# Optimization experiments

Measured on AMD Instinct MI355X. Metric: run time of the kernel, lower is better.

The kernel has to match this reference:

```python
import jax, jax.numpy as jnp
import numpy as np

B, S, DM, H, NSYN = 4, 2048, 768, 12, 4
HD = DM // H  # 64
EPS = 1e-12
SCALE = float(DM / H) ** -0.5  # 1/sqrt(head_dim)


def setup_inputs() -> dict:
    key = jax.random.key(0)
    ks = jax.random.split(key, 16)
    p = 0.02
    return {
        "hidden_states": jax.random.normal(ks[0], (B, S, DM), jnp.float32),
        "attention_mask": jnp.zeros((B, 1, 1, S), jnp.float32),
        "addi_key": jax.random.normal(ks[1], (B, NSYN, S, HD), jnp.float32),
        "addi_value": jax.random.normal(ks[2], (B, NSYN, S, HD), jnp.float32),
        "Wq": jax.random.normal(ks[3], (DM, DM), jnp.float32) * p,
        "bq": jnp.zeros((DM,), jnp.float32),
        "Wk": jax.random.normal(ks[4], (DM, DM), jnp.float32) * p,
        "bk": jnp.zeros((DM,), jnp.float32),
        "Wv": jax.random.normal(ks[5], (DM, DM), jnp.float32) * p,
        "bv": jnp.zeros((DM,), jnp.float32),
        "Wo": jax.random.normal(ks[6], (DM, DM), jnp.float32) * p,
        "bo": jnp.zeros((DM,), jnp.float32),
        "ln_g": jnp.ones((DM,), jnp.float32),
        "ln_b": jnp.zeros((DM,), jnp.float32),
    }


def _heads(x):
    # [B,S,DM] -> [B,H,S,HD]
    return x.reshape(B, S, H, HD).transpose(0, 2, 1, 3)


def reference(hidden_states, attention_mask, addi_key, addi_value,
              Wq, bq, Wk, bk, Wv, bv, Wo, bo, ln_g, ln_b):
    x = hidden_states
    q = _heads(jnp.einsum('bsi,oi->bso', x, Wq) + bq)
    k = _heads(jnp.einsum('bsi,oi->bso', x, Wk) + bk)
    v = _heads(jnp.einsum('bsi,oi->bso', x, Wv) + bv)
    # additive key/value injection on first NSYN heads
    k = k.at[:, :NSYN].add(addi_key)
    v = v.at[:, :NSYN].add(addi_value)
    scores = jnp.einsum('bhqd,bhkd->bhqk', q, k) * SCALE + attention_mask
    probs = jax.nn.softmax(scores, axis=-1)
    ctx = jnp.einsum('bhqk,bhkd->bhqd', probs, v)
    ctx = ctx.transpose(0, 2, 1, 3).reshape(B, S, DM)
    out = jnp.einsum('bsi,oi->bso', ctx, Wo) + bo
    h = out + x  # residual
    mu = jnp.mean(h, axis=-1, keepdims=True)
    var = jnp.mean((h - mu) ** 2, axis=-1, keepdims=True)
    return (h - mu) * jax.lax.rsqrt(var + EPS) * ln_g + ln_b
```

## Files before the change

kernel.cpp:

```cpp
#include <hip/hip_runtime.h>


typedef __bf16 bf16;
typedef __bf16 bf16x8 __attribute__((ext_vector_type(8)));
typedef __bf16 bf16x4 __attribute__((ext_vector_type(4)));
typedef float floatx4 __attribute__((ext_vector_type(4)));
typedef unsigned int uint2v __attribute__((ext_vector_type(2)));

#define BB 4
#define SS 2048
#define DM 768
#define HH 12
#define HD 64
#define NSYN 4
#define MM (BB*SS)
#define KK DM
#define SCALE 0.125f
#define LOG2E 1.4426950408889634f
#define QSCALE (SCALE * LOG2E)

#define N_X   ((size_t)MM * DM)
#define N_W   ((size_t)DM * DM)
#define N_M   ((size_t)BB * SS)

#if __has_builtin(__builtin_amdgcn_exp2f)
#define EXP2(x) __builtin_amdgcn_exp2f(x)
#else
#define EXP2(x) exp2f(x)
#endif

#define ASYNC16(gp, lp)                                                        \
    __builtin_amdgcn_global_load_lds(                                          \
        (const __attribute__((address_space(1))) unsigned int*)(gp),           \
        (__attribute__((address_space(3))) unsigned int*)(lp), 16, 0, 0)

static __device__ __forceinline__ void pl32_swap(unsigned int& a, unsigned int& b) {
#if __has_builtin(__builtin_amdgcn_permlane32_swap)
    uint2v r = __builtin_amdgcn_permlane32_swap(a, b, false, false);
    a = r[0]; b = r[1];
#else
    asm volatile("v_permlane32_swap_b32 %0, %1" : "+v"(a), "+v"(b));
#endif
}
static __device__ __forceinline__ void pl16_swap(unsigned int& a, unsigned int& b) {
#if __has_builtin(__builtin_amdgcn_permlane16_swap)
    uint2v r = __builtin_amdgcn_permlane16_swap(a, b, false, false);
    a = r[0]; b = r[1];
#else
    asm volatile("v_permlane16_swap_b32 %0, %1" : "+v"(a), "+v"(b));
#endif
}

__global__ __launch_bounds__(256) void cvt_kernel(
    const float* __restrict__ x,
    const float* __restrict__ Wq, const float* __restrict__ Wk,
    const float* __restrict__ Wv, const float* __restrict__ Wo,
    const float* __restrict__ mask,
    bf16* __restrict__ xb,
    bf16* __restrict__ Wqb, bf16* __restrict__ Wkb,
    bf16* __restrict__ Wvb, bf16* __restrict__ Wob,
    float* __restrict__ ml2e)
{
    const size_t nx4 = N_X / 4, nw4 = N_W / 4, nm4 = N_M / 4;
    size_t i = (size_t)blockIdx.x * blockDim.x + threadIdx.x;
    if (i >= nx4 + 4 * nw4) {
        size_t off = i - nx4 - 4 * nw4;
        if (off < nm4) {
            float4 m = *(const float4*)(mask + off * 4);
            float4 o = { m.x * LOG2E, m.y * LOG2E, m.z * LOG2E, m.w * LOG2E };
            *(float4*)(ml2e + off * 4) = o;
        }
        return;
    }
    const float* src; bf16* dst; size_t off;
    if (i < nx4)                { src = x;  dst = xb;  off = i; }
    else if (i < nx4 + nw4)     { src = Wq; dst = Wqb; off = i - nx4; }
    else if (i < nx4 + 2*nw4)   { src = Wk; dst = Wkb; off = i - nx4 - nw4; }
    else if (i < nx4 + 3*nw4)   { src = Wv; dst = Wvb; off = i - nx4 - 2*nw4; }
    else                        { src = Wo; dst = Wob; off = i - nx4 - 3*nw4; }
    float4 v = *(const float4*)(src + off * 4);
    bf16x4 o = { (bf16)v.x, (bf16)v.y, (bf16)v.z, (bf16)v.w };
    *(bf16x4*)(dst + off * 4) = o;
}

template<int ORD>
__device__ __forceinline__ void gemm_ml128_bk64(
    const bf16* __restrict__ A, const bf16* __restrict__ Bw,
    int tileM, bf16* As, bf16* Bs, floatx4 acc[2][8])
{
    const int tid  = threadIdx.x;
    const int lane = tid & 63;
    const int wave = tid >> 6;
    const int l15 = lane & 15, quad = lane >> 4;

    const int sr  = wave * 32 + (lane >> 3);
    const int scl = (lane & 7) ^ ((lane >> 3) & 7);
    const bf16* gA = A  + (size_t)(tileM * 128 + sr) * KK + scl * 8;
    const bf16* gB = Bw + (size_t)sr * KK + scl * 8;
    bf16* lA = As + (wave * 32) * 64;
    bf16* lB = Bs + (wave * 32) * 64;

    #pragma unroll
    for (int g = 0; g < 4; ++g) {
        ASYNC16(gA + (size_t)(g * 8) * KK, lA + g * 512);
        ASYNC16(gB + (size_t)(g * 8) * KK, lB + g * 512);
    }
    __syncthreads();

    for (int kt = 0; kt < KK / 64; ++kt) {
        const int cur = kt & 1;
        if (kt + 1 < KK / 64) {
            const int nb = (1 - cur) * 8192;
            #pragma unroll
            for (int g = 0; g < 4; ++g) {
                ASYNC16(gA + (kt + 1) * 64 + (size_t)(g * 8) * KK, lA + nb + g * 512);
                ASYNC16(gB + (kt + 1) * 64 + (size_t)(g * 8) * KK, lB + nb + g * 512);
            }
        }
        const bf16* cA = As + cur * 8192;
        const bf16* cB = Bs + cur * 8192;
        #pragma unroll
        for (int c = 0; c < 2; ++c) {
            const int pc = (4 * c + quad) ^ (l15 & 7);
            bf16x8 af[2];
            #pragma unroll
            for (int i = 0; i < 2; ++i)
                af[i] = *(const bf16x8*)(cA + (wave * 32 + i * 16 + l15) * 64 + pc * 8);
            #pragma unroll
            for (int j = 0; j < 8; ++j) {
                bf16x8 bfr = *(const bf16x8*)(cB + (j * 16 + l15) * 64 + pc * 8);
                #pragma unroll
                for (int i = 0; i < 2; ++i)
                    acc[i][j] = (ORD == 0)
                        ? __builtin_amdgcn_mfma_f32_16x16x32_bf16(af[i], bfr, acc[i][j], 0, 0, 0)
                        : __builtin_amdgcn_mfma_f32_16x16x32_bf16(bfr, af[i], acc[i][j], 0, 0, 0);
            }
        }
        __syncthreads();
    }
}

template<int ORD>
__device__ __forceinline__ void gemm_ml64_bk64(
    const bf16* __restrict__ A, const bf16* __restrict__ Bw,
    int tileM, int tileN, bf16* As, bf16* Bs, floatx4 acc[2][4])
{
    const int tid  = threadIdx.x;
    const int lane = tid & 63;
    const int wave = tid >> 6;
    const int l15 = lane & 15, quad = lane >> 4;

    const int srA = wave * 32 + (lane >> 3);
    const int srB = wave * 16 + (lane >> 3);
    const int scl = (lane & 7) ^ ((lane >> 3) & 7);
    const bf16* gA = A  + (size_t)(tileM * 128 + srA) * KK + scl * 8;
    const bf16* gB = Bw + (size_t)(tileN *  64 + srB) * KK + scl * 8;
    bf16* lA = As + (wave * 32) * 64;
    bf16* lB = Bs + (wave * 16) * 64;

    #pragma unroll
    for (int g = 0; g < 4; ++g) ASYNC16(gA + (size_t)(g * 8) * KK, lA + g * 512);
    #pragma unroll
    for (int g = 0; g < 2; ++g) ASYNC16(gB + (size_t)(g * 8) * KK, lB + g * 512);
    __syncthreads();

    for (int kt = 0; kt < KK / 64; ++kt) {
        const int cur = kt & 1;
        if (kt + 1 < KK / 64) {
            const int nbA = (1 - cur) * 8192;
            const int nbB = (1 - cur) * 4096;
            #pragma unroll
            for (int g = 0; g < 4; ++g)
                ASYNC16(gA + (kt + 1) * 64 + (size_t)(g * 8) * KK, lA + nbA + g * 512);
            #pragma unroll
            for (int g = 0; g < 2; ++g)
                ASYNC16(gB + (kt + 1) * 64 + (size_t)(g * 8) * KK, lB + nbB + g * 512);
        }
        const bf16* cA = As + cur * 8192;
        const bf16* cB = Bs + cur * 4096;
        #pragma unroll
        for (int c = 0; c < 2; ++c) {
            const int pc = (4 * c + quad) ^ (l15 & 7);
            bf16x8 af[2];
            #pragma unroll
            for (int i = 0; i < 2; ++i)
                af[i] = *(const bf16x8*)(cA + (wave * 32 + i * 16 + l15) * 64 + pc * 8);
            #pragma unroll
            for (int j = 0; j < 4; ++j) {
                bf16x8 bfr = *(const bf16x8*)(cB + (j * 16 + l15) * 64 + pc * 8);
                #pragma unroll
                for (int i = 0; i < 2; ++i)
                    acc[i][j] = (ORD == 0)
                        ? __builtin_amdgcn_mfma_f32_16x16x32_bf16(af[i], bfr, acc[i][j], 0, 0, 0)
                        : __builtin_amdgcn_mfma_f32_16x16x32_bf16(bfr, af[i], acc[i][j], 0, 0, 0);
            }
        }
        __syncthreads();
    }
}

__global__ __launch_bounds__(256, 2) void qkv_kernel(
    const bf16* __restrict__ xb,
    const bf16* __restrict__ Wqb, const float* __restrict__ bq,
    const bf16* __restrict__ Wkb, const float* __restrict__ bk,
    const bf16* __restrict__ Wvb, const float* __restrict__ bv,
    const float* __restrict__ addi_key, const float* __restrict__ addi_value,
    bf16* __restrict__ qbuf, bf16* __restrict__ kbuf, bf16* __restrict__ vtbuf)
{
    __shared__ __align__(16) bf16 As[2 * 128 * 64];
    __shared__ __align__(16) bf16 Bs[2 * 128 * 64];
    const int u = blockIdx.x;
    const int tileM = u & 63;
    const int tileN = u >> 6;
    const int z     = tileN / 6;
    const int tN    = tileN % 6;
    const bf16* W     = (z == 0) ? Wqb : (z == 1) ? Wkb : Wvb;
    const float* bias = (z == 0) ? bq  : (z == 1) ? bk  : bv;
    const bf16* Wrow  = W + (size_t)(tN * 128) * KK;

    floatx4 acc[2][8];
    #pragma unroll
    for (int i = 0; i < 2; ++i)
        #pragma unroll
        for (int j = 0; j < 8; ++j) { floatx4 zv = {0.f, 0.f, 0.f, 0.f}; acc[i][j] = zv; }

    const int lane = threadIdx.x & 63, wave = threadIdx.x >> 6;
    const int l15 = lane & 15, quad = lane >> 4;

    if (z == 2) {
        gemm_ml128_bk64<0>(xb, Wrow, tileM, As, Bs, acc);
        #pragma unroll
        for (int i = 0; i < 2; ++i) {
            const int sg0 = tileM * 128 + wave * 32 + i * 16 + quad * 4;
            const int b = sg0 >> 11, s0 = sg0 & 2047;
            #pragma unroll
            for (int j = 0; j < 8; ++j) {
                const int o = tN * 128 + j * 16 + l15;
                const float bv_ = bias[o];
                const int h = o >> 6, d = o & 63;
                float vv[4];
                #pragma unroll
                for (int rr = 0; rr < 4; ++rr) {
                    vv[rr] = acc[i][j][rr] + bv_;
                    if (h < NSYN)
                        vv[rr] += addi_value[(((size_t)b * NSYN + h) * SS + s0 + rr) * HD + d];
                }
                bf16x4 pk = { (bf16)vv[0], (bf16)vv[1], (bf16)vv[2], (bf16)vv[3] };
                *(bf16x4*)(vtbuf + (((size_t)b * HH + h) * HD + d) * SS + s0) = pk;
            }
        }
    } else {
        gemm_ml128_bk64<1>(xb, Wrow, tileM, As, Bs, acc);
        #pragma unroll
        for (int i = 0; i < 2; ++i) {
            const int sg = tileM * 128 + wave * 32 + i * 16 + l15;
            const int b = sg >> 11, s = sg & 2047;
            #pragma unroll
            for (int j = 0; j < 8; ++j) {
                const int o0 = tN * 128 + j * 16 + quad * 4;
                const int h = o0 >> 6, d0 = o0 & 63;
                float4 b4 = *(const float4*)(bias + o0);
                float vv[4] = { acc[i][j][0] + b4.x, acc[i][j][1] + b4.y,
                                acc[i][j][2] + b4.z, acc[i][j][3] + b4.w };
                if (z == 1 && h < NSYN) {
                    float4 a4 = *(const float4*)(addi_key +
                        (((size_t)b * NSYN + h) * SS + s) * HD + d0);
                    vv[0] += a4.x; vv[1] += a4.y; vv[2] += a4.z; vv[3] += a4.w;
                }
                if (z == 0) {
                    bf16x4 pk = { (bf16)(vv[0] * QSCALE), (bf16)(vv[1] * QSCALE),
                                  (bf16)(vv[2] * QSCALE), (bf16)(vv[3] * QSCALE) };
                    *(bf16x4*)(qbuf + (((size_t)b * HH + h) * SS + s) * HD + d0) = pk;
                } else {
                    bf16x4 pk = { (bf16)vv[0], (bf16)vv[1], (bf16)vv[2], (bf16)vv[3] };
                    *(bf16x4*)(kbuf + (((size_t)b * HH + h) * SS + s) * HD + d0) = pk;
                }
            }
        }
    }
}

__global__ __launch_bounds__(256, 3) void attn_kernel(
    const bf16* __restrict__ qbuf, const bf16* __restrict__ kbuf,
    const bf16* __restrict__ vtbuf, const float* __restrict__ ml2e,
    bf16* __restrict__ ctx)
{
    __shared__ __align__(16) bf16 Ks[2 * 64 * 64];
    __shared__ __align__(16) bf16 Vt[2 * 64 * 64];

    const int u  = blockIdx.x;
    const int bh = u % 48;
    const int qt = u / 48;
    const int b  = bh / 12;
    const int h  = bh % 12;
    const size_t bhs = ((size_t)b * HH + h) * SS * HD;
    const int tid = threadIdx.x, lane = tid & 63, wave = tid >> 6;
    const int l15 = lane & 15, quad = lane >> 4;
    const int q0 = qt * 128 + wave * 32;

    const int sr  = wave * 16 + (lane >> 3);
    const int scl = (lane & 7) ^ ((lane >> 3) & 7);
    const bf16* gK = kbuf  + bhs + (size_t)sr * HD + scl * 8;
    const bf16* gV = vtbuf + bhs + (size_t)sr * SS + scl * 8;
    bf16* lK = Ks + (wave * 16) * 64;
    bf16* lV = Vt + (wave * 16) * 64;

    bf16x8 qf[2][2];
    #pragma unroll
    for (int n = 0; n < 2; ++n)
        #pragma unroll
        for (int c = 0; c < 2; ++c)
            qf[n][c] = *(const bf16x8*)(qbuf + bhs +
                (size_t)(q0 + n * 16 + l15) * HD + c * 32 + quad * 8);

    bf16x8 ones;
    #pragma unroll
    for (int e = 0; e < 8; ++e) ones[e] = (bf16)1.0f;

    floatx4 acco[2][4];
    #pragma unroll
    for (int n = 0; n < 2; ++n)
        #pragma unroll
        for (int t = 0; t < 4; ++t) { floatx4 zv = {0.f, 0.f, 0.f, 0.f}; acco[n][t] = zv; }
    floatx4 lacc[2];
    { floatx4 zv = {0.f, 0.f, 0.f, 0.f}; lacc[0] = zv; lacc[1] = zv; }

    const float* mb = ml2e + (size_t)b * SS;

    #pragma unroll
    for (int p = 0; p < 2; ++p) {
        ASYNC16(gK + (size_t)p * 8 * HD,  lK + p * 512);
        ASYNC16(gV + (size_t)p * 8 * SS,  lV + p * 512);
    }
    __syncthreads();

    for (int kt = 0; kt < SS / 64; ++kt) {
        float4 mk4[4];
        #pragma unroll
        for (int j = 0; j < 4; ++j)
            mk4[j] = *(const float4*)(mb + kt * 64 + j * 16 + quad * 4);

        const int cur = kt & 1;
        if (kt + 1 < SS / 64) {
            const int nb = (1 - cur) * 4096;
            #pragma unroll
            for (int p = 0; p < 2; ++p) {
                ASYNC16(gK + ((size_t)(kt + 1) * 64 + p * 8) * HD, lK + nb + p * 512);
                ASYNC16(gV + (size_t)p * 8 * SS + (kt + 1) * 64,   lV + nb + p * 512);
            }
        }
        const bf16* cK = Ks + cur * 4096;
        const bf16* cV = Vt + cur * 4096;

        floatx4 sacc[2][4];
        #pragma unroll
        for (int j = 0; j < 4; ++j) {
            floatx4 mv = { mk4[j].x, mk4[j].y, mk4[j].z, mk4[j].w };
            sacc[0][j] = mv;
            sacc[1][j] = mv;
        }
        __builtin_amdgcn_s_setprio(1);
        #pragma unroll
        for (int c = 0; c < 2; ++c) {
            const int pc = (4 * c + quad) ^ (l15 & 7);
            #pragma unroll
            for (int j = 0; j < 4; ++j) {
                bf16x8 af = *(const bf16x8*)(cK + (j * 16 + l15) * 64 + pc * 8);
                #pragma unroll
                for (int n = 0; n < 2; ++n)
                    sacc[n][j] = __builtin_amdgcn_mfma_f32_16x16x32_bf16(af, qf[n][c], sacc[n][j], 0, 0, 0);
            }
        }
        __builtin_amdgcn_s_setprio(0);

        unsigned int w[2][4][2];
        #pragma unroll
        for (int j = 0; j < 4; ++j) {
            #pragma unroll
            for (int n = 0; n < 2; ++n) {
                float p0 = EXP2(sacc[n][j][0]);
                float p1 = EXP2(sacc[n][j][1]);
                float p2 = EXP2(sacc[n][j][2]);
                float p3 = EXP2(sacc[n][j][3]);
                union { bf16x4 v; unsigned int u2[2]; } pk;
                pk.v = (bf16x4){ (bf16)p0, (bf16)p1, (bf16)p2, (bf16)p3 };
                w[n][j][0] = pk.u2[0];
                w[n][j][1] = pk.u2[1];
            }
        }
        #pragma unroll
        for (int n = 0; n < 2; ++n) {
            pl32_swap(w[n][0][0], w[n][1][0]);  pl32_swap(w[n][0][1], w[n][1][1]);
            pl32_swap(w[n][2][0], w[n][3][0]);  pl32_swap(w[n][2][1], w[n][3][1]);
        }
        #pragma unroll
        for (int n = 0; n < 2; ++n) {
            pl16_swap(w[n][0][0], w[n][1][0]);  pl16_swap(w[n][0][1], w[n][1][1]);
            pl16_swap(w[n][2][0], w[n][3][0]);  pl16_swap(w[n][2][1], w[n][3][1]);
        }
        union { unsigned int u2[4]; bf16x8 v; } pb[2][2];
        #pragma unroll
        for (int n = 0; n < 2; ++n) {
            pb[n][0].u2[0] = w[n][0][0]; pb[n][0].u2[1] = w[n][0][1];
            pb[n][0].u2[2] = w[n][1][0]; pb[n][0].u2[3] = w[n][1][1];
            pb[n][1].u2[0] = w[n][2][0]; pb[n][1].u2[1] = w[n][2][1];
            pb[n][1].u2[2] = w[n][3][0]; pb[n][1].u2[3] = w[n][3][1];
        }

        __builtin_amdgcn_s_setprio(1);
        #pragma unroll
        for (int c = 0; c < 2; ++c) {
            const int pc = (4 * c + quad) ^ (l15 & 7);
            #pragma unroll
            for (int n = 0; n < 2; ++n)
                lacc[n] = __builtin_amdgcn_mfma_f32_16x16x32_bf16(ones, pb[n][c].v, lacc[n], 0, 0, 0);
            #pragma unroll
            for (int t = 0; t < 4; ++t) {
                bf16x8 af = *(const bf16x8*)(cV + (t * 16 + l15) * 64 + pc * 8);
                #pragma unroll
                for (int n = 0; n < 2; ++n)
                    acco[n][t] = __builtin_amdgcn_mfma_f32_16x16x32_bf16(af, pb[n][c].v, acco[n][t], 0, 0, 0);
            }
        }
        __builtin_amdgcn_s_setprio(0);
        __syncthreads();
    }

    #pragma unroll
    for (int n = 0; n < 2; ++n) {
        const float inv = 1.0f / lacc[n][0];
        bf16* crow = ctx + ((size_t)(b * SS + q0 + n * 16 + l15)) * DM + h * HD;
        #pragma unroll
        for (int t = 0; t < 4; ++t) {
            bf16x4 ov = { (bf16)(acco[n][t][0] * inv), (bf16)(acco[n][t][1] * inv),
                          (bf16)(acco[n][t][2] * inv), (bf16)(acco[n][t][3] * inv) };
            *(bf16x4*)(crow + t * 16 + quad * 4) = ov;
        }
    }
}

__global__ __launch_bounds__(256, 3) void oproj_kernel(
    const bf16* __restrict__ ctx, const bf16* __restrict__ Wob,
    const float* __restrict__ bo, const float* __restrict__ x,
    bf16* __restrict__ hbuf)
{
    __shared__ __align__(16) bf16 As[2 * 128 * 64];
    __shared__ __align__(16) bf16 Bs[2 * 64 * 64];
    const int u = blockIdx.x;
    const int tileM = u & 63;
    const int tileN = u >> 6;

    floatx4 acc[2][4];
    #pragma unroll
    for (int i = 0; i < 2; ++i)
        #pragma unroll
        for (int j = 0; j < 4; ++j) { floatx4 zv = {0.f, 0.f, 0.f, 0.f}; acc[i][j] = zv; }

    gemm_ml64_bk64<1>(ctx, Wob, tileM, tileN, As, Bs, acc);

    const int lane = threadIdx.x & 63, wave = threadIdx.x >> 6;
    const int l15 = lane & 15, quad = lane >> 4;
    #pragma unroll
    for (int i = 0; i < 2; ++i) {
        const int sg = tileM * 128 + wave * 32 + i * 16 + l15;
        #pragma unroll
        for (int j = 0; j < 4; ++j) {
            const int o0 = tileN * 64 + j * 16 + quad * 4;
            float4 b4 = *(const float4*)(bo + o0);
            float4 r4 = *(const float4*)(x + (size_t)sg * DM + o0);
            bf16x4 pk = { (bf16)(acc[i][j][0] + b4.x + r4.x),
                          (bf16)(acc[i][j][1] + b4.y + r4.y),
                          (bf16)(acc[i][j][2] + b4.z + r4.z),
                          (bf16)(acc[i][j][3] + b4.w + r4.w) };
            *(bf16x4*)(hbuf + (size_t)sg * DM + o0) = pk;
        }
    }
}

__global__ __launch_bounds__(256) void ln_kernel(
    const bf16* __restrict__ hbuf, const float* __restrict__ g,
    const float* __restrict__ be, float* __restrict__ out)
{
    const int row  = blockIdx.x * 4 + (threadIdx.x >> 6);
    const int lane = threadIdx.x & 63;
    const bf16* hr = hbuf + (size_t)row * DM;

    bf16x8 va = *(const bf16x8*)(hr + lane * 8);
    bf16x4 vb = *(const bf16x4*)(hr + 512 + lane * 4);
    float v[12];
    #pragma unroll
    for (int i = 0; i < 8; ++i) v[i] = (float)va[i];
    #pragma unroll
    for (int i = 0; i < 4; ++i) v[8 + i] = (float)vb[i];

    float s = 0.f;
    #pragma unroll
    for (int i = 0; i < 12; ++i) s += v[i];
    #pragma unroll
    for (int m = 1; m < 64; m <<= 1) s += __shfl_xor(s, m);
    const float mu = s * (1.0f / DM);

    float s2 = 0.f;
    #pragma unroll
    for (int i = 0; i < 12; ++i) { v[i] -= mu; s2 += v[i] * v[i]; }
    #pragma unroll
    for (int m = 1; m < 64; m <<= 1) s2 += __shfl_xor(s2, m);
    const float rsv = rsqrtf(s2 * (1.0f / DM) + 1e-12f);

    float* orow = out + (size_t)row * DM;
    const int c0 = lane * 8, c1 = 512 + lane * 4;
    float4 g0 = *(const float4*)(g + c0),     g1 = *(const float4*)(g + c0 + 4);
    float4 g2 = *(const float4*)(g + c1);
    float4 b0 = *(const float4*)(be + c0),    b1 = *(const float4*)(be + c0 + 4);
    float4 b2 = *(const float4*)(be + c1);
    float4 o0 = { v[0]*rsv*g0.x + b0.x, v[1]*rsv*g0.y + b0.y,
                  v[2]*rsv*g0.z + b0.z, v[3]*rsv*g0.w + b0.w };
    float4 o1 = { v[4]*rsv*g1.x + b1.x, v[5]*rsv*g1.y + b1.y,
                  v[6]*rsv*g1.z + b1.z, v[7]*rsv*g1.w + b1.w };
    float4 o2 = { v[8]*rsv*g2.x + b2.x, v[9]*rsv*g2.y + b2.y,
                  v[10]*rsv*g2.z + b2.z, v[11]*rsv*g2.w + b2.w };
    *(float4*)(orow + c0)     = o0;
    *(float4*)(orow + c0 + 4) = o1;
    *(float4*)(orow + c1)     = o2;
}

extern "C" void kernel_launch(void* const* d_in, const int* in_sizes, int n_in,
                              void* d_out, int out_size, void* d_ws, size_t ws_size,
                              hipStream_t stream)
{
    const float* x    = (const float*)d_in[0];
    const float* mask = (const float*)d_in[1];
    const float* akey = (const float*)d_in[2];
    const float* aval = (const float*)d_in[3];
    const float* Wq = (const float*)d_in[4];  const float* bq = (const float*)d_in[5];
    const float* Wk = (const float*)d_in[6];  const float* bk = (const float*)d_in[7];
    const float* Wv = (const float*)d_in[8];  const float* bv = (const float*)d_in[9];
    const float* Wo = (const float*)d_in[10]; const float* bo = (const float*)d_in[11];
    const float* lng = (const float*)d_in[12]; const float* lnb = (const float*)d_in[13];
    float* outp = (float*)d_out;

    const size_t nqkv = (size_t)BB * HH * SS * HD;
    char* ws = (char*)d_ws;
    bf16*  xb   = (bf16*)ws;   ws += N_X  * sizeof(bf16);
    bf16*  Wqb  = (bf16*)ws;   ws += N_W  * sizeof(bf16);
    bf16*  Wkb  = (bf16*)ws;   ws += N_W  * sizeof(bf16);
    bf16*  Wvb  = (bf16*)ws;   ws += N_W  * sizeof(bf16);
    bf16*  Wob  = (bf16*)ws;   ws += N_W  * sizeof(bf16);
    float* ml2e = (float*)ws;  ws += N_M  * sizeof(float);
    bf16*  qbuf = (bf16*)ws;   ws += nqkv * sizeof(bf16);
    bf16*  kbuf = (bf16*)ws;   ws += nqkv * sizeof(bf16);
    bf16*  vtbuf= (bf16*)ws;   ws += nqkv * sizeof(bf16);
    bf16*  ctxb = (bf16*)ws;   ws += nqkv * sizeof(bf16);
    bf16*  hbuf = (bf16*)ws;   ws += nqkv * sizeof(bf16);

    const size_t ncvt = (N_X + 4 * N_W + N_M) / 4;
    const int cvt_blocks = (int)((ncvt + 255) / 256);
    cvt_kernel<<<cvt_blocks, 256, 0, stream>>>(x, Wq, Wk, Wv, Wo, mask,
                                               xb, Wqb, Wkb, Wvb, Wob, ml2e);

    qkv_kernel<<<1152, 256, 0, stream>>>(xb, Wqb, bq, Wkb, bk, Wvb, bv, akey, aval,
                                         qbuf, kbuf, vtbuf);
    attn_kernel<<<768, 256, 0, stream>>>(qbuf, kbuf, vtbuf, ml2e, ctxb);
    oproj_kernel<<<768, 256, 0, stream>>>(ctxb, Wob, bo, x, hbuf);
    ln_kernel<<<MM / 4, 256, 0, stream>>>(hbuf, lng, lnb, outp);
}
```

Baseline: 270.8 us.

## Load weight fragments directly from global memory in QKV and output-projection GEMMs

The projection GEMMs stop staging the weight tile in LDS and instead read the B fragments for the MFMAs straight from global memory each k-step, relying on L2/L1 reuse across blocks. This halves LDS use per block, so the launch bounds are raised to allow four blocks per CU. The cost is global-load latency sitting directly in the MFMA inner loop with no prefetch, so the math may stall waiting on memory, and the higher occupancy target can cause register spills.

```diff
diff --git a/kernel.cpp b/kernel.cpp
--- a/kernel.cpp
+++ b/kernel.cpp
@@ -84,9 +84,9 @@
 }
 
 template<int ORD>
-__device__ __forceinline__ void gemm_ml128_bk64(
+__device__ __forceinline__ void gemm_ml128_breg(
     const bf16* __restrict__ A, const bf16* __restrict__ Bw,
-    int tileM, bf16* As, bf16* Bs, floatx4 acc[2][8])
+    int tileM, bf16* As, floatx4 acc[2][8])
 {
     const int tid  = threadIdx.x;
     const int lane = tid & 63;
@@ -95,16 +95,11 @@
 
     const int sr  = wave * 32 + (lane >> 3);
     const int scl = (lane & 7) ^ ((lane >> 3) & 7);
-    const bf16* gA = A  + (size_t)(tileM * 128 + sr) * KK + scl * 8;
-    const bf16* gB = Bw + (size_t)sr * KK + scl * 8;
+    const bf16* gA = A + (size_t)(tileM * 128 + sr) * KK + scl * 8;
     bf16* lA = As + (wave * 32) * 64;
-    bf16* lB = Bs + (wave * 32) * 64;
-
-    #pragma unroll
-    for (int g = 0; g < 4; ++g) {
-        ASYNC16(gA + (size_t)(g * 8) * KK, lA + g * 512);
-        ASYNC16(gB + (size_t)(g * 8) * KK, lB + g * 512);
-    }
+
+    #pragma unroll
+    for (int g = 0; g < 4; ++g) ASYNC16(gA + (size_t)(g * 8) * KK, lA + g * 512);
     __syncthreads();
 
     for (int kt = 0; kt < KK / 64; ++kt) {
@@ -112,13 +107,11 @@
         if (kt + 1 < KK / 64) {
             const int nb = (1 - cur) * 8192;
             #pragma unroll
-            for (int g = 0; g < 4; ++g) {
+            for (int g = 0; g < 4; ++g)
                 ASYNC16(gA + (kt + 1) * 64 + (size_t)(g * 8) * KK, lA + nb + g * 512);
-                ASYNC16(gB + (kt + 1) * 64 + (size_t)(g * 8) * KK, lB + nb + g * 512);
-            }
         }
         const bf16* cA = As + cur * 8192;
-        const bf16* cB = Bs + cur * 8192;
+        const bf16* gB = Bw + kt * 64;
         #pragma unroll
         for (int c = 0; c < 2; ++c) {
             const int pc = (4 * c + quad) ^ (l15 & 7);
@@ -128,7 +121,8 @@
                 af[i] = *(const bf16x8*)(cA + (wave * 32 + i * 16 + l15) * 64 + pc * 8);
             #pragma unroll
             for (int j = 0; j < 8; ++j) {
-                bf16x8 bfr = *(const bf16x8*)(cB + (j * 16 + l15) * 64 + pc * 8);
+                bf16x8 bfr = *(const bf16x8*)(gB + (size_t)(j * 16 + l15) * KK
+                                              + c * 32 + quad * 8);
                 #pragma unroll
                 for (int i = 0; i < 2; ++i)
                     acc[i][j] = (ORD == 0)
@@ -141,43 +135,34 @@
 }
 
 template<int ORD>
-__device__ __forceinline__ void gemm_ml64_bk64(
+__device__ __forceinline__ void gemm_ml64_breg(
     const bf16* __restrict__ A, const bf16* __restrict__ Bw,
-    int tileM, int tileN, bf16* As, bf16* Bs, floatx4 acc[2][4])
+    int tileM, int tileN, bf16* As, floatx4 acc[2][4])
 {
     const int tid  = threadIdx.x;
     const int lane = tid & 63;
     const int wave = tid >> 6;
     const int l15 = lane & 15, quad = lane >> 4;
 
-    const int srA = wave * 32 + (lane >> 3);
-    const int srB = wave * 16 + (lane >> 3);
+    const int sr  = wave * 32 + (lane >> 3);
     const int scl = (lane & 7) ^ ((lane >> 3) & 7);
-    const bf16* gA = A  + (size_t)(tileM * 128 + srA) * KK + scl * 8;
-    const bf16* gB = Bw + (size_t)(tileN *  64 + srB) * KK + scl * 8;
+    const bf16* gA = A + (size_t)(tileM * 128 + sr) * KK + scl * 8;
     bf16* lA = As + (wave * 32) * 64;
-    bf16* lB = Bs + (wave * 16) * 64;
 
     #pragma unroll
     for (int g = 0; g < 4; ++g) ASYNC16(gA + (size_t)(g * 8) * KK, lA + g * 512);
-    #pragma unroll
-    for (int g = 0; g < 2; ++g) ASYNC16(gB + (size_t)(g * 8) * KK, lB + g * 512);
     __syncthreads();
 
     for (int kt = 0; kt < KK / 64; ++kt) {
         const int cur = kt & 1;
         if (kt + 1 < KK / 64) {
-            const int nbA = (1 - cur) * 8192;
-            const int nbB = (1 - cur) * 4096;
+            const int nb = (1 - cur) * 8192;
             #pragma unroll
             for (int g = 0; g < 4; ++g)
-                ASYNC16(gA + (kt + 1) * 64 + (size_t)(g * 8) * KK, lA + nbA + g * 512);
-            #pragma unroll
-            for (int g = 0; g < 2; ++g)
-                ASYNC16(gB + (kt + 1) * 64 + (size_t)(g * 8) * KK, lB + nbB + g * 512);
+                ASYNC16(gA + (kt + 1) * 64 + (size_t)(g * 8) * KK, lA + nb + g * 512);
         }
         const bf16* cA = As + cur * 8192;
-        const bf16* cB = Bs + cur * 4096;
+        const bf16* gB = Bw + (size_t)(tileN * 64) * KK + kt * 64;
         #pragma unroll
         for (int c = 0; c < 2; ++c) {
             const int pc = (4 * c + quad) ^ (l15 & 7);
@@ -187,7 +172,8 @@
                 af[i] = *(const bf16x8*)(cA + (wave * 32 + i * 16 + l15) * 64 + pc * 8);
             #pragma unroll
             for (int j = 0; j < 4; ++j) {
-                bf16x8 bfr = *(const bf16x8*)(cB + (j * 16 + l15) * 64 + pc * 8);
+                bf16x8 bfr = *(const bf16x8*)(gB + (size_t)(j * 16 + l15) * KK
+                                              + c * 32 + quad * 8);
                 #pragma unroll
                 for (int i = 0; i < 2; ++i)
                     acc[i][j] = (ORD == 0)
@@ -199,7 +185,7 @@
     }
 }
 
-__global__ __launch_bounds__(256, 2) void qkv_kernel(
+__global__ __launch_bounds__(256, 4) void qkv_kernel(
     const bf16* __restrict__ xb,
     const bf16* __restrict__ Wqb, const float* __restrict__ bq,
     const bf16* __restrict__ Wkb, const float* __restrict__ bk,
@@ -208,7 +194,6 @@
     bf16* __restrict__ qbuf, bf16* __restrict__ kbuf, bf16* __restrict__ vtbuf)
 {
     __shared__ __align__(16) bf16 As[2 * 128 * 64];
-    __shared__ __align__(16) bf16 Bs[2 * 128 * 64];
     const int u = blockIdx.x;
     const int tileM = u & 63;
     const int tileN = u >> 6;
@@ -228,7 +213,7 @@
     const int l15 = lane & 15, quad = lane >> 4;
 
     if (z == 2) {
-        gemm_ml128_bk64<0>(xb, Wrow, tileM, As, Bs, acc);
+        gemm_ml128_breg<0>(xb, Wrow, tileM, As, acc);
         #pragma unroll
         for (int i = 0; i < 2; ++i) {
             const int sg0 = tileM * 128 + wave * 32 + i * 16 + quad * 4;
@@ -250,7 +235,7 @@
             }
         }
     } else {
-        gemm_ml128_bk64<1>(xb, Wrow, tileM, As, Bs, acc);
+        gemm_ml128_breg<1>(xb, Wrow, tileM, As, acc);
         #pragma unroll
         for (int i = 0; i < 2; ++i) {
             const int sg = tileM * 128 + wave * 32 + i * 16 + l15;
@@ -439,13 +424,12 @@
     }
 }
 
-__global__ __launch_bounds__(256, 3) void oproj_kernel(
+__global__ __launch_bounds__(256, 4) void oproj_kernel(
     const bf16* __restrict__ ctx, const bf16* __restrict__ Wob,
     const float* __restrict__ bo, const float* __restrict__ x,
     bf16* __restrict__ hbuf)
 {
     __shared__ __align__(16) bf16 As[2 * 128 * 64];
-    __shared__ __align__(16) bf16 Bs[2 * 64 * 64];
     const int u = blockIdx.x;
     const int tileM = u & 63;
     const int tileN = u >> 6;
@@ -456,7 +440,7 @@
         #pragma unroll
         for (int j = 0; j < 4; ++j) { floatx4 zv = {0.f, 0.f, 0.f, 0.f}; acc[i][j] = zv; }
 
-    gemm_ml64_bk64<1>(ctx, Wob, tileM, tileN, As, Bs, acc);
+    gemm_ml64_breg<1>(ctx, Wob, tileM, tileN, As, acc);
 
     const int lane = threadIdx.x & 63, wave = threadIdx.x >> 6;
     const int l15 = lane & 15, quad = lane >> 4;
```

Result: slower. 383.6 us (+41.7%).
